# Kernel optimization log

Hardware: AMD Instinct MI355X
Metric: run time of the kernel (lower is better)

The kernel has to match this reference:

```python
import jax, jax.numpy as jnp
import numpy as np

B, D0 = 1, 32
C = [32, 16, 16, 16]
DN = ('NDHWC', 'DHWIO', 'NDHWC')


def setup_inputs() -> dict:
    key = jax.random.key(0)
    ks = jax.random.split(key, 16)
    w = lambda k, s: jax.random.normal(k, s, jnp.float32) * 0.05
    occ0 = jax.random.bernoulli(ks[0], 0.3, (B, D0, D0, D0))
    x = jax.random.normal(ks[1], (B, D0, D0, D0, C[0]), jnp.float32) * occ0[..., None]
    gt0 = jax.random.bernoulli(ks[2], 0.3, (B, D0, D0, D0))
    gt1 = jax.random.bernoulli(ks[3], 0.3, (B, 2 * D0, 2 * D0, 2 * D0))
    gt2 = jax.random.bernoulli(ks[4], 0.3, (B, 4 * D0, 4 * D0, 4 * D0))
    return dict(
        x=x, occ0=occ0, gt0=gt0, gt1=gt1, gt2=gt2,
        w_conv0=w(ks[5], (3, 3, 3, C[0], C[1])), b_conv0=w(ks[6], (C[1],)),
        w_cls0=w(ks[7], (3, 3, 3, C[1], 1)), b_cls0=w(ks[8], (1,)),
        w_up1=w(ks[9], (2, 2, 2, C[1], C[2])), b_up1=w(ks[10], (C[2],)),
        w_conv1=w(ks[11], (3, 3, 3, C[2], C[2])), b_conv1=w(ks[12], (C[2],)),
        w_cls1=w(ks[13], (3, 3, 3, C[2], 1)), b_cls1=w(ks[14], (1,)),
        w_up2=w(jax.random.fold_in(key, 100), (2, 2, 2, C[2], C[3])), b_up2=w(jax.random.fold_in(key, 101), (C[3],)),
        w_conv2=w(jax.random.fold_in(key, 102), (3, 3, 3, C[3], C[3])), b_conv2=w(jax.random.fold_in(key, 103), (C[3],)),
        w_cls2=w(jax.random.fold_in(key, 104), (3, 3, 3, C[3], 1)), b_cls2=w(jax.random.fold_in(key, 105), (1,)),
        nums0=8192, nums1=32768, nums2=131072)


def conv3x3(x, w, b, occ):
    # stride-1 sparse conv == dense conv masked to existing coords
    y = jax.lax.conv_general_dilated(x, w, (1, 1, 1), 'SAME', dimension_numbers=DN)
    return (y + b) * occ[..., None].astype(y.dtype)


def up2x(x, w, b, occ):
    # generative transpose conv: every occupied voxel emits all 8 children
    y = jax.lax.conv_transpose(x, w, (2, 2, 2), 'VALID', dimension_numbers=DN)
    occ_up = jnp.repeat(jnp.repeat(jnp.repeat(occ, 2, 1), 2, 2), 2, 3)
    return (y + b) * occ_up[..., None].astype(y.dtype), occ_up


def prune(feats, occ, cls_logits, gt, k):
    # istopk over existing voxels, OR-ed with ground-truth membership (training=True)
    b = feats.shape[0]
    logits = jnp.where(occ, cls_logits[..., 0], -jnp.inf).reshape(b, -1)
    _, idx = jax.lax.top_k(logits, k)
    topk = jnp.zeros(logits.shape, bool).at[jnp.arange(b)[:, None], idx].set(True)
    mask = (topk.reshape(occ.shape) & occ) | (gt & occ)
    return feats * mask[..., None].astype(feats.dtype), mask


def hp_decoder(x, occ0, gt0, gt1, gt2,
               w_conv0, b_conv0, w_cls0, b_cls0,
               w_up1, b_up1, w_conv1, b_conv1, w_cls1, b_cls1,
               w_up2, b_up2, w_conv2, b_conv2, w_cls2, b_cls2,
               nums0, nums1, nums2):
    occ = occ0
    out = jax.nn.relu(conv3x3(x, w_conv0, b_conv0, occ))
    cls0 = conv3x3(out, w_cls0, b_cls0, occ)
    out, occ = prune(out, occ, cls0, gt0, nums0)
    h, occ = up2x(out, w_up1, b_up1, occ)
    out = jax.nn.relu(conv3x3(jax.nn.relu(h), w_conv1, b_conv1, occ))
    cls1 = conv3x3(out, w_cls1, b_cls1, occ)
    out, occ = prune(out, occ, cls1, gt1, nums1)
    h, occ = up2x(out, w_up2, b_up2, occ)
    out = jax.nn.relu(conv3x3(jax.nn.relu(h), w_conv2, b_conv2, occ))
    cls2 = conv3x3(out, w_cls2, b_cls2, occ)
    out, occ = prune(out, occ, cls2, gt2, nums2)
    return cls0, cls1, cls2, out


def reference(x, occ0, gt0, gt1, gt2,
              w_conv0, b_conv0, w_cls0, b_cls0,
              w_up1, b_up1, w_conv1, b_conv1, w_cls1, b_cls1,
              w_up2, b_up2, w_conv2, b_conv2, w_cls2, b_cls2,
              nums0, nums1, nums2):
    return hp_decoder(x, occ0, gt0, gt1, gt2,
                      w_conv0, b_conv0, w_cls0, b_cls0,
                      w_up1, b_up1, w_conv1, b_conv1, w_cls1, b_cls1,
                      w_up2, b_up2, w_conv2, b_conv2, w_cls2, b_cls2,
                      nums0, nums1, nums2)
```

## Files before the change

### kernel.cpp

```cpp
#include <hip/hip_runtime.h>
#include <stdint.h>


#define N0 32768
#define N1 262144
#define N2 2097152

#define OFF_CLS0 0L
#define OFF_CLS1 32768L
#define OFF_CLS2 294912L
#define OFF_OUT  2392064L

#define O_FLAGS 0UL
#define O_STATE 256UL
#define O_TIE   512UL
#define O_HIST1 66048UL
#define O_HIST2 328192UL
#define O_OCC0  590336UL
#define O_OCC1  623104UL
#define O_OCC2  885248UL
#define O_MASK0 2982400UL
#define O_MASK1 3015168UL
#define O_BCNT  3277312UL
#define O_SEL   5374464UL
#define O_KEYS  7471616UL
#define O_FEAT0 15860224UL
#define O_HR1   17957376UL
#define O_FEAT1 34734592UL
#define O_HR2   51511808UL
#define O_FEAT2 185729536UL

#define TIE_CAP 16000

__device__ __forceinline__ float ldf(const void* p, long i, int bf) {
    if (bf) {
        uint16_t h = ((const uint16_t*)p)[i];
        return __uint_as_float(((uint32_t)h) << 16);
    }
    return ((const float*)p)[i];
}
__device__ __forceinline__ int ldb(const void* p, long i, int m) {
    switch (m) {
        case 0: return ((const int*)p)[i] != 0;
        case 1: return ((const uint8_t*)p)[i] != 0;
        case 2: { uint16_t h = ((const uint16_t*)p)[i]; return (h & 0x7FFF) != 0; }
        case 4: return ((const long long*)p)[i] != 0;
        default: { float f = ((const float*)p)[i]; return f != 0.0f; }
    }
}
__device__ __forceinline__ float rndb(float f, int en) {
    if (!en) return f;
    uint32_t u = __float_as_uint(f);
    u += 0x7FFFu + ((u >> 16) & 1u);
    u &= 0xFFFF0000u;
    return __uint_as_float(u);
}
__device__ __forceinline__ void stf(void* p, long i, float v, int bf) {
    if (bf) {
        uint32_t u = __float_as_uint(v);
        u += 0x7FFFu + ((u >> 16) & 1u);
        ((uint16_t*)p)[i] = (uint16_t)(u >> 16);
    } else {
        ((float*)p)[i] = v;
    }
}
__device__ __forceinline__ uint32_t fkey(float f) {
    f = f + 0.0f;
    uint32_t u = __float_as_uint(f);
    return (u & 0x80000000u) ? ~u : (u | 0x80000000u);
}

__global__ void k_fzero(int* flags) {
    int t = threadIdx.x;
    if (t < 16) flags[8 + t] = 0;
}
__global__ void k_fscan(const void* x, const void* gt2, int* flags) {
    int* cnt = flags + 8;
    __shared__ int lc[8];
    int t = threadIdx.x;
    if (t < 8) lc[t] = 0;
    __syncthreads();
    long gid = (long)blockIdx.x * blockDim.x + threadIdx.x;
    long gstride = (long)gridDim.x * blockDim.x;
    int ltiny = 0;
    const uint32_t* xu = (const uint32_t*)x;
    for (long i = gid; i < 524288; i += gstride) {
        uint32_t u = xu[i];
        uint32_t e = (u >> 23) & 0xFFu;
        if (e == 0u && (u & 0x7FFFFFu) != 0u) ltiny++;
    }
    int l1off = 0, l1any = 0, l3f = 0, l84 = 0;
    const uint8_t* g = (const uint8_t*)gt2;
    for (long i = gid; i < 2097152; i += gstride) {
        uint8_t b = g[i];
        if (b == 1u) {
            l1any++;
            if ((i & 3) != 0) l1off++;
            if ((i & 7) == 4) l84++;
        }
        if (b == 0x3Fu && (i & 3) == 1) l3f++;
    }
    if (ltiny) atomicAdd(&lc[0], ltiny);
    if (l1off) atomicAdd(&lc[1], l1off);
    if (l1any) atomicAdd(&lc[2], l1any);
    if (l3f)   atomicAdd(&lc[3], l3f);
    if (l84)   atomicAdd(&lc[4], l84);
    __syncthreads();
    if (t < 5 && lc[t]) atomicAdd(&cnt[t], lc[t]);
}
__global__ void k_ffinal(int* flags) {
    if (threadIdx.x != 0 || blockIdx.x != 0) return;
    const int* cnt = flags + 8;
    flags[0] = (cnt[0] > 8) ? 1 : 0;
    int bm;
    if (cnt[1] > 8)       bm = 1;
    else if (cnt[2] > 8)  bm = (cnt[4] > 8) ? 0 : 4;
    else if (cnt[3] > 8)  bm = 2;
    else                  bm = 3;
    flags[1] = bm;
}

__global__ void k_zout(void* dout, long out_elems, const int* flags) {
    long bytes = out_elems * (flags[0] ? 2 : 4);
    long n16 = bytes >> 4;
    uint4 z = make_uint4(0, 0, 0, 0);
    uint4* p = (uint4*)dout;
    long stride = (long)gridDim.x * blockDim.x;
    for (long i = (long)blockIdx.x * blockDim.x + threadIdx.x; i < n16; i += stride)
        p[i] = z;
}

__global__ void k_occ0(const void* occraw, uint8_t* occ, const int* flags) {
    long v = (long)blockIdx.x * blockDim.x + threadIdx.x;
    if (v >= N0) return;
    occ[v] = (uint8_t)ldb(occraw, v, flags[1]);
}

__global__ void k_xcast(const void* x, float* xf, const int* flags) {
    long i = (long)blockIdx.x * blockDim.x + threadIdx.x;
    if (i >= (long)N0 * 32) return;
    xf[i] = ldf(x, i, flags[0]);
}

__global__ void k_cnt(const uint8_t* __restrict__ occ, long N,
                      int* __restrict__ bcnt, uint8_t* maskz) {
    long v = (long)blockIdx.x * 256 + threadIdx.x;
    int a = (v < N) && occ[v];
    if (maskz && v < N) maskz[v] = 0;
    unsigned long long m = __ballot(a != 0);
    __shared__ int wsum[4];
    int lane = threadIdx.x & 63, wid = threadIdx.x >> 6;
    if (lane == 0) wsum[wid] = (int)__popcll(m);
    __syncthreads();
    if (threadIdx.x == 0)
        bcnt[blockIdx.x] = wsum[0] + wsum[1] + wsum[2] + wsum[3];
}
__global__ void k_scanb(int* __restrict__ bcnt, int nb, int* cnt) {
    __shared__ int tsum[256];
    __shared__ int tpre[257];
    int t = threadIdx.x;
    int ch = (nb + 255) / 256;
    int lo = t * ch, hi = min(lo + ch, nb);
    int s = 0;
    for (int i = lo; i < hi; i++) s += bcnt[i];
    tsum[t] = s;
    __syncthreads();
    if (t == 0) {
        int run = 0;
        for (int j = 0; j < 256; j++) { tpre[j] = run; run += tsum[j]; }
        tpre[256] = run;
        cnt[0] = run;
    }
    __syncthreads();
    int run = tpre[t];
    for (int i = lo; i < hi; i++) { int x = bcnt[i]; bcnt[i] = run; run += x; }
}
__global__ void k_fill(const uint8_t* __restrict__ occ, long N,
                       const int* __restrict__ bcnt, int* __restrict__ list) {
    long v = (long)blockIdx.x * 256 + threadIdx.x;
    int a = (v < N) && occ[v];
    unsigned long long m = __ballot(a != 0);
    __shared__ int wsum[4];
    int lane = threadIdx.x & 63, wid = threadIdx.x >> 6;
    if (lane == 0) wsum[wid] = (int)__popcll(m);
    __syncthreads();
    int base = bcnt[blockIdx.x];
    for (int w = 0; w < wid; w++) base += wsum[w];
    if (a) list[base + (int)__popcll(m & ((1ull << lane) - 1ull))] = (int)v;
}

template <int CIN, int D>
__global__ void k_sconv16(const float* __restrict__ xin, const void* w, const void* bias,
                          const uint8_t* __restrict__ occ, const int* __restrict__ list,
                          const int* __restrict__ cnt, float* __restrict__ out,
                          const int* __restrict__ flags) {
    __shared__ float wl[27 * CIN * 16 + 16];
    const int n = cnt[0];
    if (blockIdx.x * 128 >= n) return;
    const int bf = flags[0];
    for (int i = threadIdx.x; i < 27 * CIN * 16; i += 256) wl[i] = ldf(w, i, bf);
    if (threadIdx.x < 16) wl[27 * CIN * 16 + threadIdx.x] = ldf(bias, threadIdx.x, bf);
    __syncthreads();
    int gid = blockIdx.x * 256 + threadIdx.x;
    int i = gid >> 1;
    if (i >= n) return;
    const int half = gid & 1;
    int v = list[i];
    int wd = v % D, hh = (v / D) % D, dd = v / (D * D);
    uint32_t nbm = 0u;
    {
        int t = 0;
#pragma unroll
        for (int kd = 0; kd < 3; kd++)
#pragma unroll
            for (int kh = 0; kh < 3; kh++)
#pragma unroll
                for (int kw = 0; kw < 3; kw++, t++) {
                    int d2 = dd + kd - 1, h2 = hh + kh - 1, w2 = wd + kw - 1;
                    int ok = (int)((unsigned)d2 < (unsigned)D) &
                             (int)((unsigned)h2 < (unsigned)D) &
                             (int)((unsigned)w2 < (unsigned)D);
                    int nv = v + (kd - 1) * D * D + (kh - 1) * D + (kw - 1);
                    int nvc = ok ? nv : v;
                    nbm |= ((uint32_t)((int)occ[nvc] & ok)) << t;
                }
    }
    float acc[8];
#pragma unroll
    for (int co = 0; co < 8; co++) acc[co] = 0.0f;
    int t = 0;
    for (int kd = 0; kd < 3; kd++) {
        for (int kh = 0; kh < 3; kh++) {
            for (int kw = 0; kw < 3; kw++, t++) {
                if (!((nbm >> t) & 1u)) continue;
                long nv = (long)v + (kd - 1) * (D * D) + (kh - 1) * D + (kw - 1);
                const float4* xp = (const float4*)(xin + nv * CIN);
                const float* wp = &wl[((kd * 3 + kh) * 3 + kw) * CIN * 16 + half * 8];
#pragma unroll
                for (int c4 = 0; c4 < CIN / 4; c4++) {
                    float4 x4 = xp[c4];
                    const float* wq = wp + c4 * 64;
#pragma unroll
                    for (int co = 0; co < 8; co++) acc[co] += x4.x * wq[co];
#pragma unroll
                    for (int co = 0; co < 8; co++) acc[co] += x4.y * wq[16 + co];
#pragma unroll
                    for (int co = 0; co < 8; co++) acc[co] += x4.z * wq[32 + co];
#pragma unroll
                    for (int co = 0; co < 8; co++) acc[co] += x4.w * wq[48 + co];
                }
            }
        }
    }
    float* op = out + (long)v * 16 + half * 8;
    const float* bp = &wl[27 * CIN * 16 + half * 8];
#pragma unroll
    for (int co = 0; co < 8; co++) {
        float val = rndb(acc[co], bf);
        val = rndb(val + bp[co], bf);
        op[co] = fmaxf(val, 0.0f);
    }
}

template <int D>
__global__ void k_scls(const float* __restrict__ feat, const void* w, const void* bias,
                       const uint8_t* __restrict__ occ, const int* __restrict__ list,
                       const int* __restrict__ cnt, void* dout, long ooff,
                       uint32_t* __restrict__ keyl, const int* __restrict__ flags) {
    __shared__ float wl[27 * 16 + 1];
    const int n = cnt[0];
    if (blockIdx.x * 256 >= n) return;
    const int bf = flags[0];
    for (int i = threadIdx.x; i < 27 * 16; i += 256) wl[i] = ldf(w, i, bf);
    if (threadIdx.x == 0) wl[432] = ldf(bias, 0, bf);
    __syncthreads();
    int i = blockIdx.x * 256 + threadIdx.x;
    if (i >= n) return;
    int v = list[i];
    int wd = v % D, hh = (v / D) % D, dd = v / (D * D);
    uint32_t nbm = 0u;
    {
        int t = 0;
#pragma unroll
        for (int kd = 0; kd < 3; kd++)
#pragma unroll
            for (int kh = 0; kh < 3; kh++)
#pragma unroll
                for (int kw = 0; kw < 3; kw++, t++) {
                    int d2 = dd + kd - 1, h2 = hh + kh - 1, w2 = wd + kw - 1;
                    int ok = (int)((unsigned)d2 < (unsigned)D) &
                             (int)((unsigned)h2 < (unsigned)D) &
                             (int)((unsigned)w2 < (unsigned)D);
                    int nv = v + (kd - 1) * D * D + (kh - 1) * D + (kw - 1);
                    int nvc = ok ? nv : v;
                    nbm |= ((uint32_t)((int)occ[nvc] & ok)) << t;
                }
    }
    float acc = 0.0f;
    int t = 0;
    for (int kd = 0; kd < 3; kd++) {
        for (int kh = 0; kh < 3; kh++) {
            for (int kw = 0; kw < 3; kw++, t++) {
                if (!((nbm >> t) & 1u)) continue;
                long nv = (long)v + (kd - 1) * (D * D) + (kh - 1) * D + (kw - 1);
                const float4* xp = (const float4*)(feat + nv * 16);
                const float* wp = &wl[((kd * 3 + kh) * 3 + kw) * 16];
                float4 a0 = xp[0], a1 = xp[1], a2 = xp[2], a3 = xp[3];
                acc += a0.x * wp[0] + a0.y * wp[1] + a0.z * wp[2] + a0.w * wp[3];
                acc += a1.x * wp[4] + a1.y * wp[5] + a1.z * wp[6] + a1.w * wp[7];
                acc += a2.x * wp[8] + a2.y * wp[9] + a2.z * wp[10] + a2.w * wp[11];
                acc += a3.x * wp[12] + a3.y * wp[13] + a3.z * wp[14] + a3.w * wp[15];
            }
        }
    }
    float val = rndb(acc, bf);
    val = rndb(val + wl[432], bf);
    stf(dout, ooff + v, val, bf);
    keyl[i] = fkey(val);
}

template <int Dp>
__global__ void k_sup(const float* __restrict__ featp, const void* w, const void* bias,
                      const int* __restrict__ list, const int* __restrict__ cnt,
                      float* __restrict__ hrelu, const int* __restrict__ flags) {
    __shared__ float wl[2048 + 16];
    const int n = cnt[0];
    if (blockIdx.x * 256 >= n) return;
    const int bf = flags[0];
    for (int i = threadIdx.x; i < 2048; i += 256) wl[i] = ldf(w, i, bf);
    if (threadIdx.x < 16) wl[2048 + threadIdx.x] = ldf(bias, threadIdx.x, bf);
    __syncthreads();
    int i = blockIdx.x * 256 + threadIdx.x;
    if (i >= n) return;
    int v = list[i];
    const int D = Dp * 2;
    int wd = v % D, hh = (v / D) % D, dd = v / (D * D);
    const float4* xp = (const float4*)(featp +
        ((long)((dd >> 1) * Dp + (hh >> 1)) * Dp + (wd >> 1)) * 16);
    int a = 1 - (dd & 1), b2 = 1 - (hh & 1), c = 1 - (wd & 1);
    const float* wp = &wl[((a * 2 + b2) * 2 + c) * 256];
    float acc[16];
#pragma unroll
    for (int co = 0; co < 16; co++) acc[co] = 0.0f;
#pragma unroll
    for (int c4 = 0; c4 < 4; c4++) {
        float4 x4 = xp[c4];
        const float* wq = wp + c4 * 64;
#pragma unroll
        for (int co = 0; co < 16; co++) acc[co] += x4.x * wq[co];
#pragma unroll
        for (int co = 0; co < 16; co++) acc[co] += x4.y * wq[16 + co];
#pragma unroll
        for (int co = 0; co < 16; co++) acc[co] += x4.z * wq[32 + co];
#pragma unroll
        for (int co = 0; co < 16; co++) acc[co] += x4.w * wq[48 + co];
    }
    float* op = hrelu + (long)v * 16;
#pragma unroll
    for (int co = 0; co < 16; co++) {
        float val = rndb(acc[co], bf);
        val = rndb(val + wl[2048 + co], bf);
        op[co] = fmaxf(val, 0.0f);
    }
}

template <int Dp>
__global__ void k_expand(const uint8_t* __restrict__ maskp, uint8_t* __restrict__ occc) {
    const int D = Dp * 2;
    long v = (long)blockIdx.x * blockDim.x + threadIdx.x;
    if (v >= (long)D * D * D) return;
    int wd = (int)(v % D), hh = (int)((v / D) % D), dd = (int)(v / ((long)D * D));
    occc[v] = maskp[((long)(dd >> 1) * Dp + (hh >> 1)) * Dp + (wd >> 1)];
}

__global__ void k_hzero(uint32_t* hist1, int* state) {
    int i = blockIdx.x * blockDim.x + threadIdx.x;
    if (i < 65536) hist1[i] = 0u;
    if (i < 16) state[i] = 0;
}
__global__ void k_hist1(const uint32_t* __restrict__ keyl, const int* cnt,
                        uint32_t* __restrict__ hist) {
    __shared__ uint32_t lh[32768];
    const int n = cnt[0];
    for (int j = threadIdx.x; j < 32768; j += 256) lh[j] = 0u;
    __syncthreads();
    const int stride = gridDim.x * 256;
    for (int i = blockIdx.x * 256 + threadIdx.x; i < n; i += stride) {
        uint32_t bin = keyl[i] >> 16;
        atomicAdd(&lh[bin >> 1], 1u << ((bin & 1u) << 4));
    }
    __syncthreads();
    for (int j = threadIdx.x; j < 32768; j += 256) {
        uint32_t p = lh[j];
        if (p) {
            uint32_t lo = p & 0xFFFFu, hi = p >> 16;
            if (lo) atomicAdd(&hist[2 * j], lo);
            if (hi) atomicAdd(&hist[2 * j + 1], hi);
        }
    }
}
__global__ void k_scan1(const uint32_t* hist, const void* kptr, const int* cnt,
                        int* state, uint32_t* hist2) {
    __shared__ uint32_t part[256];
    int t = threadIdx.x;
    uint32_t s = 0;
    for (int j = 0; j < 256; j++) s += hist[t * 256 + j];
    part[t] = s;
    for (int i = t; i < 65536; i += 256) hist2[i] = 0u;
    __syncthreads();
    if (t == 0) {
        uint32_t k = (uint32_t)((const int*)kptr)[0];
        uint32_t total = (uint32_t)cnt[0];
        if (k >= total) {
            state[0] = -1;
            state[3] = 0;
            state[4] = 0;
            state[5] = 0;
            return;
        }
        uint32_t cum = 0, cab = 0;
        int B = 0;
        for (int c = 255; c >= 0; c--) {
            if (cum + part[c] >= k) {
                uint32_t cc = cum;
                for (int b = c * 256 + 255; b >= c * 256; b--) {
                    uint32_t h = hist[b];
                    if (cc + h >= k) { B = b; cab = cc; break; }
                    cc += h;
                }
                break;
            }
            cum += part[c];
        }
        state[0] = B;
        state[1] = (int)cab;
        state[2] = (int)(k - cab);
    }
}
__global__ void k_hist2(const uint32_t* __restrict__ keyl, const int* cnt,
                        const int* state, uint32_t* __restrict__ hist2) {
    if (state[0] < 0) return;
    __shared__ uint32_t lh[32768];
    const int n = cnt[0];
    const int B = state[0];
    for (int j = threadIdx.x; j < 32768; j += 256) lh[j] = 0u;
    __syncthreads();
    const int stride = gridDim.x * 256;
    for (int i = blockIdx.x * 256 + threadIdx.x; i < n; i += stride) {
        uint32_t key = keyl[i];
        if ((int)(key >> 16) == B) {
            uint32_t bin = key & 0xFFFFu;
            atomicAdd(&lh[bin >> 1], 1u << ((bin & 1u) << 4));
        }
    }
    __syncthreads();
    for (int j = threadIdx.x; j < 32768; j += 256) {
        uint32_t p = lh[j];
        if (p) {
            uint32_t lo = p & 0xFFFFu, hi = p >> 16;
            if (lo) atomicAdd(&hist2[2 * j], lo);
            if (hi) atomicAdd(&hist2[2 * j + 1], hi);
        }
    }
}
__global__ void k_scan2(const uint32_t* hist2, int* state) {
    __shared__ uint32_t part[256];
    int t = threadIdx.x;
    if (state[0] < 0) return;
    uint32_t s = 0;
    for (int j = 0; j < 256; j++) s += hist2[t * 256 + j];
    part[t] = s;
    __syncthreads();
    if (t == 0) {
        uint32_t krem = (uint32_t)state[2];
        uint32_t cum = 0, cl = 0;
        int L = 0;
        for (int c = 255; c >= 0; c--) {
            if (cum + part[c] >= krem) {
                uint32_t cc = cum;
                for (int b = c * 256 + 255; b >= c * 256; b--) {
                    uint32_t h = hist2[b];
                    if (cc + h >= krem) { L = b; cl = cc; break; }
                    cc += h;
                }
                break;
            }
            cum += part[c];
        }
        uint32_t K = ((uint32_t)state[0] << 16) | (uint32_t)L;
        state[3] = (int)K;
        state[4] = (int)(krem - cl);
        state[5] = 0;
    }
}
__global__ void k_mark(const uint32_t* __restrict__ keyl, const int* __restrict__ list,
                       const int* cnt, int* state, uint8_t* __restrict__ sel, int* tiel) {
    int n = cnt[0];
    int i = blockIdx.x * 256 + threadIdx.x;
    uint32_t K = (uint32_t)state[3];
    int v = 0, isTie = 0;
    if (i < n) {
        uint32_t key = keyl[i];
        v = list[i];
        sel[v] = (key > K) ? (uint8_t)1 : (uint8_t)0;
        isTie = (key == K && K != 0u);
    }
    unsigned long long m = __ballot(isTie != 0);
    if (m) {
        int lane = threadIdx.x & 63;
        int leader = __ffsll((unsigned long long)m) - 1;
        int base = 0;
        if (lane == leader) base = atomicAdd(&state[5], (int)__popcll(m));
        base = __shfl(base, leader, 64);
        if (isTie) {
            int pos = base + (int)__popcll(m & ((1ull << lane) - 1ull));
            if (pos < TIE_CAP) tiel[pos] = v;
        }
    }
}
__global__ void k_ties(const int* state, const int* tiel, uint8_t* sel) {
    __shared__ int lst[TIE_CAP];
    int T = state[5];
    if (T > TIE_CAP) T = TIE_CAP;
    int need = state[4];
    if (need <= 0 || T == 0) return;
    for (int i = threadIdx.x; i < T; i += blockDim.x) lst[i] = tiel[i];
    __syncthreads();
    for (int e = threadIdx.x; e < T; e += blockDim.x) {
        int idx = lst[e], r = 0;
        for (int j = 0; j < T; j++) r += (lst[j] < idx) ? 1 : 0;
        if (r < need) sel[idx] = 1;
    }
}
__global__ void k_sapply(const uint8_t* __restrict__ sel, const int* __restrict__ list,
                         const int* cnt, const void* gt, uint8_t* __restrict__ mask,
                         const int* flags) {
    int n = cnt[0];
    int i = blockIdx.x * 256 + threadIdx.x;
    if (i >= n) return;
    int v = list[i];
    mask[v] = (uint8_t)(sel[v] || ldb(gt, v, flags[1]));
}
__global__ void k_sapply_out(const uint8_t* __restrict__ sel, const int* __restrict__ list,
                             const int* cnt, const void* gt, const float* __restrict__ feat,
                             void* dout, const int* flags) {
    int n = cnt[0];
    int i = blockIdx.x * 256 + threadIdx.x;
    if (i >= n) return;
    int v = list[i];
    if (!(sel[v] || ldb(gt, v, flags[1]))) return;
    const int bf = flags[0];
    long base = OFF_OUT + (long)v * 16;
    const float* fp = feat + (long)v * 16;
#pragma unroll
    for (int co = 0; co < 16; co++) stf(dout, base + co, fp[co], bf);
}

extern "C" void kernel_launch(void* const* d_in, const int* in_sizes, int n_in,
                              void* d_out, int out_size, void* d_ws, size_t ws_size,
                              hipStream_t stream) {
    char* ws = (char*)d_ws;
    int* flags = (int*)(ws + O_FLAGS);
    int* cnt = flags + 32;
    int* state = (int*)(ws + O_STATE);
    int* tiel = (int*)(ws + O_TIE);
    uint32_t* h1 = (uint32_t*)(ws + O_HIST1);
    uint32_t* h2 = (uint32_t*)(ws + O_HIST2);
    uint8_t* occ0 = (uint8_t*)(ws + O_OCC0);
    uint8_t* occ1 = (uint8_t*)(ws + O_OCC1);
    uint8_t* occ2 = (uint8_t*)(ws + O_OCC2);
    uint8_t* mask0 = (uint8_t*)(ws + O_MASK0);
    uint8_t* mask1 = (uint8_t*)(ws + O_MASK1);
    int* bcnt = (int*)(ws + O_BCNT);
    uint8_t* sel = (uint8_t*)(ws + O_SEL);
    uint32_t* keyl = (uint32_t*)(ws + O_KEYS);
    float* feat0 = (float*)(ws + O_FEAT0);
    float* hr1 = (float*)(ws + O_HR1);
    float* feat1 = (float*)(ws + O_FEAT1);
    float* hr2 = (float*)(ws + O_HR2);
    float* feat2 = (float*)(ws + O_FEAT2);
    int* list0 = (int*)(ws + O_HR1);
    int* list1 = (int*)(ws + O_HR2);
    int* list2 = (int*)(ws + O_HR1);
    float* xf = (float*)(ws + O_HR2 + (4UL << 20));

    k_fzero<<<1, 64, 0, stream>>>(flags);
    k_fscan<<<512, 256, 0, stream>>>(d_in[0], d_in[4], flags);
    k_ffinal<<<1, 64, 0, stream>>>(flags);
    k_zout<<<2048, 256, 0, stream>>>(d_out, (long)out_size, flags);
    k_occ0<<<N0 / 256, 256, 0, stream>>>(d_in[1], occ0, flags);
    k_xcast<<<(N0 * 32) / 256, 256, 0, stream>>>(d_in[0], xf, flags);

    k_cnt<<<N0 / 256, 256, 0, stream>>>(occ0, N0, bcnt, mask0);
    k_scanb<<<1, 256, 0, stream>>>(bcnt, N0 / 256, cnt);
    k_fill<<<N0 / 256, 256, 0, stream>>>(occ0, N0, bcnt, list0);
    k_sconv16<32, 32><<<(2 * N0) / 256, 256, 0, stream>>>(xf, d_in[5], d_in[6], occ0,
                                                          list0, cnt, feat0, flags);
    k_scls<32><<<N0 / 256, 256, 0, stream>>>(feat0, d_in[7], d_in[8], occ0, list0,
                                             cnt, d_out, OFF_CLS0, keyl, flags);
    k_hzero<<<256, 256, 0, stream>>>(h1, state);
    k_hist1<<<256, 256, 0, stream>>>(keyl, cnt, h1);
    k_scan1<<<1, 256, 0, stream>>>(h1, d_in[21], cnt, state, h2);
    k_hist2<<<256, 256, 0, stream>>>(keyl, cnt, state, h2);
    k_scan2<<<1, 256, 0, stream>>>(h2, state);
    k_mark<<<N0 / 256, 256, 0, stream>>>(keyl, list0, cnt, state, sel, tiel);
    k_ties<<<1, 1024, 0, stream>>>(state, tiel, sel);
    k_sapply<<<N0 / 256, 256, 0, stream>>>(sel, list0, cnt, d_in[2], mask0, flags);

    k_expand<32><<<N1 / 256, 256, 0, stream>>>(mask0, occ1);
    k_cnt<<<N1 / 256, 256, 0, stream>>>(occ1, N1, bcnt, mask1);
    k_scanb<<<1, 256, 0, stream>>>(bcnt, N1 / 256, cnt);
    k_fill<<<N1 / 256, 256, 0, stream>>>(occ1, N1, bcnt, list1);
    k_sup<32><<<N1 / 256, 256, 0, stream>>>(feat0, d_in[9], d_in[10], list1, cnt,
                                            hr1, flags);
    k_sconv16<16, 64><<<(2 * N1) / 256, 256, 0, stream>>>(hr1, d_in[11], d_in[12], occ1,
                                                          list1, cnt, feat1, flags);
    k_scls<64><<<N1 / 256, 256, 0, stream>>>(feat1, d_in[13], d_in[14], occ1, list1,
                                             cnt, d_out, OFF_CLS1, keyl, flags);
    k_hzero<<<256, 256, 0, stream>>>(h1, state);
    k_hist1<<<256, 256, 0, stream>>>(keyl, cnt, h1);
    k_scan1<<<1, 256, 0, stream>>>(h1, d_in[22], cnt, state, h2);
    k_hist2<<<256, 256, 0, stream>>>(keyl, cnt, state, h2);
    k_scan2<<<1, 256, 0, stream>>>(h2, state);
    k_mark<<<N1 / 256, 256, 0, stream>>>(keyl, list1, cnt, state, sel, tiel);
    k_ties<<<1, 1024, 0, stream>>>(state, tiel, sel);
    k_sapply<<<N1 / 256, 256, 0, stream>>>(sel, list1, cnt, d_in[3], mask1, flags);

    k_expand<64><<<N2 / 256, 256, 0, stream>>>(mask1, occ2);
    k_cnt<<<N2 / 256, 256, 0, stream>>>(occ2, N2, bcnt, (uint8_t*)0);
    k_scanb<<<1, 256, 0, stream>>>(bcnt, N2 / 256, cnt);
    k_fill<<<N2 / 256, 256, 0, stream>>>(occ2, N2, bcnt, list2);
    k_sup<64><<<N2 / 256, 256, 0, stream>>>(feat1, d_in[15], d_in[16], list2, cnt,
                                            hr2, flags);
    k_sconv16<16, 128><<<(2 * N2) / 256, 256, 0, stream>>>(hr2, d_in[17], d_in[18], occ2,
                                                           list2, cnt, feat2, flags);
    k_scls<128><<<N2 / 256, 256, 0, stream>>>(feat2, d_in[19], d_in[20], occ2, list2,
                                              cnt, d_out, OFF_CLS2, keyl, flags);
    k_hzero<<<256, 256, 0, stream>>>(h1, state);
    k_hist1<<<256, 256, 0, stream>>>(keyl, cnt, h1);
    k_scan1<<<1, 256, 0, stream>>>(h1, d_in[23], cnt, state, h2);
    k_hist2<<<256, 256, 0, stream>>>(keyl, cnt, state, h2);
    k_scan2<<<1, 256, 0, stream>>>(h2, state);
    k_mark<<<N2 / 256, 256, 0, stream>>>(keyl, list2, cnt, state, sel, tiel);
    k_ties<<<1, 1024, 0, stream>>>(state, tiel, sel);
    k_sapply_out<<<N2 / 256, 256, 0, stream>>>(sel, list2, cnt, d_in[4], feat2,
                                               d_out, flags);
}
```

Before: 886.4 us.

## Fuse occupancy, count, histogram-zero and prune-apply kernels; split cls conv across lanes

Several small kernels are merged to cut launch count and extra passes over voxel arrays. The occ0 conversion is folded into the block count. The 2x expansion is folded into counting, and histogram zeroing moves into the list fill. Marking now writes the mask (OR ground truth) directly, and at the last level it writes the output features, which removes the separate sel array and apply kernels. The cls conv now uses two lanes per voxel, each taking alternate kernel taps, combined with a shuffle-reduce. This doubles the threads for that gather-bound stage at the cost of some lane divergence. The per-level reset of state that k_hzero used to do is dropped, so correctness relies on other kernels resetting those fields.

```diff
diff --git a/kernel.cpp b/kernel.cpp
--- a/kernel.cpp
+++ b/kernel.cpp
@@ -130,23 +130,38 @@
         p[i] = z;
 }
 
-__global__ void k_occ0(const void* occraw, uint8_t* occ, const int* flags) {
-    long v = (long)blockIdx.x * blockDim.x + threadIdx.x;
-    if (v >= N0) return;
-    occ[v] = (uint8_t)ldb(occraw, v, flags[1]);
-}
-
 __global__ void k_xcast(const void* x, float* xf, const int* flags) {
     long i = (long)blockIdx.x * blockDim.x + threadIdx.x;
     if (i >= (long)N0 * 32) return;
     xf[i] = ldf(x, i, flags[0]);
 }
 
-__global__ void k_cnt(const uint8_t* __restrict__ occ, long N,
-                      int* __restrict__ bcnt, uint8_t* maskz) {
+__global__ void k_occ0cnt(const void* occraw, uint8_t* occ, const int* flags,
+                          int* __restrict__ bcnt, uint8_t* maskz) {
     long v = (long)blockIdx.x * 256 + threadIdx.x;
-    int a = (v < N) && occ[v];
-    if (maskz && v < N) maskz[v] = 0;
+    int a = (v < N0) ? ldb(occraw, v, flags[1]) : 0;
+    if (v < N0) { occ[v] = (uint8_t)a; maskz[v] = 0; }
+    unsigned long long m = __ballot(a != 0);
+    __shared__ int wsum[4];
+    int lane = threadIdx.x & 63, wid = threadIdx.x >> 6;
+    if (lane == 0) wsum[wid] = (int)__popcll(m);
+    __syncthreads();
+    if (threadIdx.x == 0)
+        bcnt[blockIdx.x] = wsum[0] + wsum[1] + wsum[2] + wsum[3];
+}
+template <int Dp>
+__global__ void k_expcnt(const uint8_t* __restrict__ maskp, uint8_t* __restrict__ occc,
+                         int* __restrict__ bcnt, uint8_t* maskz) {
+    const int D = Dp * 2;
+    long v = (long)blockIdx.x * 256 + threadIdx.x;
+    const long N = (long)D * D * D;
+    int a = 0;
+    if (v < N) {
+        int wd = (int)(v % D), hh = (int)((v / D) % D), dd = (int)(v / ((long)D * D));
+        a = maskp[((long)(dd >> 1) * Dp + (hh >> 1)) * Dp + (wd >> 1)];
+        occc[v] = (uint8_t)a;
+        if (maskz) maskz[v] = 0;
+    }
     unsigned long long m = __ballot(a != 0);
     __shared__ int wsum[4];
     int lane = threadIdx.x & 63, wid = threadIdx.x >> 6;
@@ -176,8 +191,10 @@
     for (int i = lo; i < hi; i++) { int x = bcnt[i]; bcnt[i] = run; run += x; }
 }
 __global__ void k_fill(const uint8_t* __restrict__ occ, long N,
-                       const int* __restrict__ bcnt, int* __restrict__ list) {
+                       const int* __restrict__ bcnt, int* __restrict__ list,
+                       uint32_t* __restrict__ h1z) {
     long v = (long)blockIdx.x * 256 + threadIdx.x;
+    for (long j = v; j < 65536; j += (long)gridDim.x * 256) h1z[j] = 0u;
     int a = (v < N) && occ[v];
     unsigned long long m = __ballot(a != 0);
     __shared__ int wsum[4];
@@ -269,13 +286,15 @@
                        uint32_t* __restrict__ keyl, const int* __restrict__ flags) {
     __shared__ float wl[27 * 16 + 1];
     const int n = cnt[0];
-    if (blockIdx.x * 256 >= n) return;
+    if (blockIdx.x * 128 >= n) return;
     const int bf = flags[0];
     for (int i = threadIdx.x; i < 27 * 16; i += 256) wl[i] = ldf(w, i, bf);
     if (threadIdx.x == 0) wl[432] = ldf(bias, 0, bf);
     __syncthreads();
-    int i = blockIdx.x * 256 + threadIdx.x;
+    int gid = blockIdx.x * 256 + threadIdx.x;
+    int i = gid >> 1;
     if (i >= n) return;
+    const int half = gid & 1;
     int v = list[i];
     int wd = v % D, hh = (v / D) % D, dd = v / (D * D);
     uint32_t nbm = 0u;
@@ -301,6 +320,7 @@
     for (int kd = 0; kd < 3; kd++) {
         for (int kh = 0; kh < 3; kh++) {
             for (int kw = 0; kw < 3; kw++, t++) {
+                if ((t & 1) != half) continue;
                 if (!((nbm >> t) & 1u)) continue;
                 long nv = (long)v + (kd - 1) * (D * D) + (kh - 1) * D + (kw - 1);
                 const float4* xp = (const float4*)(feat + nv * 16);
@@ -313,10 +333,13 @@
             }
         }
     }
-    float val = rndb(acc, bf);
-    val = rndb(val + wl[432], bf);
-    stf(dout, ooff + v, val, bf);
-    keyl[i] = fkey(val);
+    acc += __shfl_xor(acc, 1, 64);
+    if (half == 0) {
+        float val = rndb(acc, bf);
+        val = rndb(val + wl[432], bf);
+        stf(dout, ooff + v, val, bf);
+        keyl[i] = fkey(val);
+    }
 }
 
 template <int Dp>
@@ -364,20 +387,6 @@
     }
 }
 
-template <int Dp>
-__global__ void k_expand(const uint8_t* __restrict__ maskp, uint8_t* __restrict__ occc) {
-    const int D = Dp * 2;
-    long v = (long)blockIdx.x * blockDim.x + threadIdx.x;
-    if (v >= (long)D * D * D) return;
-    int wd = (int)(v % D), hh = (int)((v / D) % D), dd = (int)(v / ((long)D * D));
-    occc[v] = maskp[((long)(dd >> 1) * Dp + (hh >> 1)) * Dp + (wd >> 1)];
-}
-
-__global__ void k_hzero(uint32_t* hist1, int* state) {
-    int i = blockIdx.x * blockDim.x + threadIdx.x;
-    if (i < 65536) hist1[i] = 0u;
-    if (i < 16) state[i] = 0;
-}
 __global__ void k_hist1(const uint32_t* __restrict__ keyl, const int* cnt,
                         uint32_t* __restrict__ hist) {
     __shared__ uint32_t lh[32768];
@@ -493,8 +502,9 @@
         state[5] = 0;
     }
 }
-__global__ void k_mark(const uint32_t* __restrict__ keyl, const int* __restrict__ list,
-                       const int* cnt, int* state, uint8_t* __restrict__ sel, int* tiel) {
+__global__ void k_markm(const uint32_t* __restrict__ keyl, const int* __restrict__ list,
+                        const int* cnt, int* state, const void* gt,
+                        uint8_t* __restrict__ mask, int* tiel, const int* flags) {
     int n = cnt[0];
     int i = blockIdx.x * 256 + threadIdx.x;
     uint32_t K = (uint32_t)state[3];
@@ -502,7 +512,7 @@
     if (i < n) {
         uint32_t key = keyl[i];
         v = list[i];
-        sel[v] = (key > K) ? (uint8_t)1 : (uint8_t)0;
+        mask[v] = (uint8_t)((key > K) || ldb(gt, v, flags[1]));
         isTie = (key == K && K != 0u);
     }
     unsigned long long m = __ballot(isTie != 0);
@@ -518,7 +528,7 @@
         }
     }
 }
-__global__ void k_ties(const int* state, const int* tiel, uint8_t* sel) {
+__global__ void k_tiesm(const int* state, const int* tiel, uint8_t* mask) {
     __shared__ int lst[TIE_CAP];
     int T = state[5];
     if (T > TIE_CAP) T = TIE_CAP;
@@ -529,31 +539,61 @@
     for (int e = threadIdx.x; e < T; e += blockDim.x) {
         int idx = lst[e], r = 0;
         for (int j = 0; j < T; j++) r += (lst[j] < idx) ? 1 : 0;
-        if (r < need) sel[idx] = 1;
-    }
-}
-__global__ void k_sapply(const uint8_t* __restrict__ sel, const int* __restrict__ list,
-                         const int* cnt, const void* gt, uint8_t* __restrict__ mask,
-                         const int* flags) {
+        if (r < need) mask[idx] = 1;
+    }
+}
+__global__ void k_marko(const uint32_t* __restrict__ keyl, const int* __restrict__ list,
+                        const int* cnt, int* state, const void* gt,
+                        const float* __restrict__ feat, void* dout, int* tiel,
+                        const int* flags) {
     int n = cnt[0];
     int i = blockIdx.x * 256 + threadIdx.x;
-    if (i >= n) return;
-    int v = list[i];
-    mask[v] = (uint8_t)(sel[v] || ldb(gt, v, flags[1]));
-}
-__global__ void k_sapply_out(const uint8_t* __restrict__ sel, const int* __restrict__ list,
-                             const int* cnt, const void* gt, const float* __restrict__ feat,
-                             void* dout, const int* flags) {
-    int n = cnt[0];
-    int i = blockIdx.x * 256 + threadIdx.x;
-    if (i >= n) return;
-    int v = list[i];
-    if (!(sel[v] || ldb(gt, v, flags[1]))) return;
+    uint32_t K = (uint32_t)state[3];
+    int v = 0, isTie = 0;
     const int bf = flags[0];
-    long base = OFF_OUT + (long)v * 16;
-    const float* fp = feat + (long)v * 16;
-#pragma unroll
-    for (int co = 0; co < 16; co++) stf(dout, base + co, fp[co], bf);
+    if (i < n) {
+        uint32_t key = keyl[i];
+        v = list[i];
+        if ((key > K) || ldb(gt, v, flags[1])) {
+            long base = OFF_OUT + (long)v * 16;
+            const float* fp = feat + (long)v * 16;
+#pragma unroll
+            for (int co = 0; co < 16; co++) stf(dout, base + co, fp[co], bf);
+        }
+        isTie = (key == K && K != 0u);
+    }
+    unsigned long long m = __ballot(isTie != 0);
+    if (m) {
+        int lane = threadIdx.x & 63;
+        int leader = __ffsll((unsigned long long)m) - 1;
+        int base = 0;
+        if (lane == leader) base = atomicAdd(&state[5], (int)__popcll(m));
+        base = __shfl(base, leader, 64);
+        if (isTie) {
+            int pos = base + (int)__popcll(m & ((1ull << lane) - 1ull));
+            if (pos < TIE_CAP) tiel[pos] = v;
+        }
+    }
+}
+__global__ void k_tieso(const int* state, const int* tiel,
+                        const float* __restrict__ feat, void* dout, const int* flags) {
+    __shared__ int lst[TIE_CAP];
+    int T = state[5];
+    if (T > TIE_CAP) T = TIE_CAP;
+    int need = state[4];
+    if (need <= 0 || T == 0) return;
+    const int bf = flags[0];
+    for (int i = threadIdx.x; i < T; i += blockDim.x) lst[i] = tiel[i];
+    __syncthreads();
+    for (int e = threadIdx.x; e < T; e += blockDim.x) {
+        int idx = lst[e], r = 0;
+        for (int j = 0; j < T; j++) r += (lst[j] < idx) ? 1 : 0;
+        if (r < need) {
+            long base = OFF_OUT + (long)idx * 16;
+            const float* fp = feat + (long)idx * 16;
+            for (int co = 0; co < 16; co++) stf(dout, base + co, fp[co], bf);
+        }
+    }
 }
 
 extern "C" void kernel_launch(void* const* d_in, const int* in_sizes, int n_in,
@@ -572,7 +612,6 @@
     uint8_t* mask0 = (uint8_t*)(ws + O_MASK0);
     uint8_t* mask1 = (uint8_t*)(ws + O_MASK1);
     int* bcnt = (int*)(ws + O_BCNT);
-    uint8_t* sel = (uint8_t*)(ws + O_SEL);
     uint32_t* keyl = (uint32_t*)(ws + O_KEYS);
     float* feat0 = (float*)(ws + O_FEAT0);
     float* hr1 = (float*)(ws + O_HR1);
@@ -588,61 +627,57 @@
     k_fscan<<<512, 256, 0, stream>>>(d_in[0], d_in[4], flags);
     k_ffinal<<<1, 64, 0, stream>>>(flags);
     k_zout<<<2048, 256, 0, stream>>>(d_out, (long)out_size, flags);
-    k_occ0<<<N0 / 256, 256, 0, stream>>>(d_in[1], occ0, flags);
     k_xcast<<<(N0 * 32) / 256, 256, 0, stream>>>(d_in[0], xf, flags);
 
-    k_cnt<<<N0 / 256, 256, 0, stream>>>(occ0, N0, bcnt, mask0);
+    k_occ0cnt<<<N0 / 256, 256, 0, stream>>>(d_in[1], occ0, flags, bcnt, mask0);
     k_scanb<<<1, 256, 0, stream>>>(bcnt, N0 / 256, cnt);
-    k_fill<<<N0 / 256, 256, 0, stream>>>(occ0, N0, bcnt, list0);
+    k_fill<<<N0 / 256, 256, 0, stream>>>(occ0, N0, bcnt, list0, h1);
     k_sconv16<32, 32><<<(2 * N0) / 256, 256, 0, stream>>>(xf, d_in[5], d_in[6], occ0,
                                                           list0, cnt, feat0, flags);
-    k_scls<32><<<N0 / 256, 256, 0, stream>>>(feat0, d_in[7], d_in[8], occ0, list0,
-                                             cnt, d_out, OFF_CLS0, keyl, flags);
-    k_hzero<<<256, 256, 0, stream>>>(h1, state);
+    k_scls<32><<<(2 * N0) / 256, 256, 0, stream>>>(feat0, d_in[7], d_in[8], occ0, list0,
+                                                   cnt, d_out, OFF_CLS0, keyl, flags);
     k_hist1<<<256, 256, 0, stream>>>(keyl, cnt, h1);
     k_scan1<<<1, 256, 0, stream>>>(h1, d_in[21], cnt, state, h2);
     k_hist2<<<256, 256, 0, stream>>>(keyl, cnt, state, h2);
     k_scan2<<<1, 256, 0, stream>>>(h2, state);
-    k_mark<<<N0 / 256, 256, 0, stream>>>(keyl, list0, cnt, state, sel, tiel);
-    k_ties<<<1, 1024, 0, stream>>>(state, tiel, sel);
-    k_sapply<<<N0 / 256, 256, 0, stream>>>(sel, list0, cnt, d_in[2], mask0, flags);
-
-    k_expand<32><<<N1 / 256, 256, 0, stream>>>(mask0, occ1);
-    k_cnt<<<N1 / 256, 256, 0, stream>>>(occ1, N1, bcnt, mask1);
+    k_markm<<<N0 / 256, 256, 0, stream>>>(keyl, list0, cnt, state, d_in[2], mask0,
+                                          tiel, flags);
+    k_tiesm<<<1, 1024, 0, stream>>>(state, tiel, mask0);
+
+    k_expcnt<32><<<N1 / 256, 256, 0, stream>>>(mask0, occ1, bcnt, mask1);
     k_scanb<<<1, 256, 0, stream>>>(bcnt, N1 / 256, cnt);
-    k_fill<<<N1 / 256, 256, 0, stream>>>(occ1, N1, bcnt, list1);
+    k_fill<<<N1 / 256, 256, 0, stream>>>(occ1, N1, bcnt, list1, h1);
     k_sup<32><<<N1 / 256, 256, 0, stream>>>(feat0, d_in[9], d_in[10], list1, cnt,
                                             hr1, flags);
     k_sconv16<16, 64><<<(2 * N1) / 256, 256, 0, stream>>>(hr1, d_in[11], d_in[12], occ1,
                                                           list1, cnt, feat1, flags);
-    k_scls<64><<<N1 / 256, 256, 0, stream>>>(feat1, d_in[13], d_in[14], occ1, list1,
-                                             cnt, d_out, OFF_CLS1, keyl, flags);
-    k_hzero<<<256, 256, 0, stream>>>(h1, state);
+    k_scls<64><<<(2 * N1) / 256, 256, 0, stream>>>(feat1, d_in[13], d_in[14], occ1,
+                                                   list1, cnt, d_out, OFF_CLS1, keyl,
+                                                   flags);
     k_hist1<<<256, 256, 0, stream>>>(keyl, cnt, h1);
     k_scan1<<<1, 256, 0, stream>>>(h1, d_in[22], cnt, state, h2);
     k_hist2<<<256, 256, 0, stream>>>(keyl, cnt, state, h2);
     k_scan2<<<1, 256, 0, stream>>>(h2, state);
-    k_mark<<<N1 / 256, 256, 0, stream>>>(keyl, list1, cnt, state, sel, tiel);
-    k_ties<<<1, 1024, 0, stream>>>(state, tiel, sel);
-    k_sapply<<<N1 / 256, 256, 0, stream>>>(sel, list1, cnt, d_in[3], mask1, flags);
-
-    k_expand<64><<<N2 / 256, 256, 0, stream>>>(mask1, occ2);
-    k_cnt<<<N2 / 256, 256, 0, stream>>>(occ2, N2, bcnt, (uint8_t*)0);
+    k_markm<<<N1 / 256, 256, 0, stream>>>(keyl, list1, cnt, state, d_in[3], mask1,
+                                          tiel, flags);
+    k_tiesm<<<1, 1024, 0, stream>>>(state, tiel, mask1);
+
+    k_expcnt<64><<<N2 / 256, 256, 0, stream>>>(mask1, occ2, bcnt, (uint8_t*)0);
     k_scanb<<<1, 256, 0, stream>>>(bcnt, N2 / 256, cnt);
-    k_fill<<<N2 / 256, 256, 0, stream>>>(occ2, N2, bcnt, list2);
+    k_fill<<<N2 / 256, 256, 0, stream>>>(occ2, N2, bcnt, list2, h1);
     k_sup<64><<<N2 / 256, 256, 0, stream>>>(feat1, d_in[15], d_in[16], list2, cnt,
                                             hr2, flags);
-    k_sconv16<16, 128><<<(2 * N2) / 256, 256, 0, stream>>>(hr2, d_in[17], d_in[18], occ2,
-                                                           list2, cnt, feat2, flags);
-    k_scls<128><<<N2 / 256, 256, 0, stream>>>(feat2, d_in[19], d_in[20], occ2, list2,
-                                              cnt, d_out, OFF_CLS2, keyl, flags);
-    k_hzero<<<256, 256, 0, stream>>>(h1, state);
+    k_sconv16<16, 128><<<(2 * N2) / 256, 256, 0, stream>>>(hr2, d_in[17], d_in[18],
+                                                           occ2, list2, cnt, feat2,
+                                                           flags);
+    k_scls<128><<<(2 * N2) / 256, 256, 0, stream>>>(feat2, d_in[19], d_in[20], occ2,
+                                                    list2, cnt, d_out, OFF_CLS2, keyl,
+                                                    flags);
     k_hist1<<<256, 256, 0, stream>>>(keyl, cnt, h1);
     k_scan1<<<1, 256, 0, stream>>>(h1, d_in[23], cnt, state, h2);
     k_hist2<<<256, 256, 0, stream>>>(keyl, cnt, state, h2);
     k_scan2<<<1, 256, 0, stream>>>(h2, state);
-    k_mark<<<N2 / 256, 256, 0, stream>>>(keyl, list2, cnt, state, sel, tiel);
-    k_ties<<<1, 1024, 0, stream>>>(state, tiel, sel);
-    k_sapply_out<<<N2 / 256, 256, 0, stream>>>(sel, list2, cnt, d_in[4], feat2,
-                                               d_out, flags);
-}
+    k_marko<<<N2 / 256, 256, 0, stream>>>(keyl, list2, cnt, state, d_in[4], feat2,
+                                          d_out, tiel, flags);
+    k_tieso<<<1, 1024, 0, stream>>>(state, tiel, feat2, d_out, flags);
+}
```

Measured after the change: 867.0 us. 2.2% less time.
